# Kernel tuning notes

Measured on AMD Instinct MI355X. Metric: run time of the kernel, lower is better.

Reference implementation:

```python
import jax, jax.numpy as jnp
import numpy as np

EMBED_DIM = 1024
NUM_HEADS = 16
HEAD_DIM = EMBED_DIM // NUM_HEADS


def setup_inputs() -> dict:
    key = jax.random.key(0)
    ks = jax.random.split(key, 6)
    s = 1.0 / np.sqrt(EMBED_DIM)
    x = jax.random.normal(ks[0], (2, 2048, EMBED_DIM), dtype=jnp.float32)
    # torch Linear weights are [out, in]; y = x @ W.T
    Wq = jax.random.uniform(ks[1], (EMBED_DIM, EMBED_DIM), jnp.float32, -s, s)
    Wk = jax.random.uniform(ks[2], (EMBED_DIM, EMBED_DIM), jnp.float32, -s, s)
    Wv = jax.random.uniform(ks[3], (EMBED_DIM, EMBED_DIM), jnp.float32, -s, s)
    Wo = jax.random.uniform(ks[4], (EMBED_DIM, EMBED_DIM), jnp.float32, -s, s)
    bo = jax.random.uniform(ks[5], (EMBED_DIM,), jnp.float32, -s, s)
    return {"x": x, "Wq": Wq, "Wk": Wk, "Wv": Wv, "Wo": Wo, "bo": bo}


def reference(x, Wq, Wk, Wv, Wo, bo):
    B, T, C = x.shape
    H, D = NUM_HEADS, HEAD_DIM
    # projections (torch Linear: x @ W.T)
    Q = (x @ Wq.T).reshape(B, T, H, D).transpose(0, 2, 1, 3)  # [B,H,T,D]
    K = (x @ Wk.T).reshape(B, T, H, D).transpose(0, 2, 1, 3)
    V = (x @ Wv.T).reshape(B, T, H, D).transpose(0, 2, 1, 3)
    scores = jnp.einsum('bhqd,bhkd->bhqk', Q, K) / jnp.sqrt(jnp.float32(D))
    causal = jnp.tril(jnp.ones((T, T), dtype=bool))
    scores = jnp.where(causal, scores, -jnp.inf)
    weights = jax.nn.softmax(scores, axis=-1)  # dropout=0.0 (eval): identity
    out = jnp.einsum('bhqk,bhkd->bhqd', weights, V)
    out = out.transpose(0, 2, 1, 3).reshape(B, T, C)
    return out @ Wo.T + bo
```

## Files before the change

### kernel.cpp

```cpp
#include <hip/hip_runtime.h>
#include <stdint.h>

typedef unsigned short u16;
typedef __bf16 bf16x4 __attribute__((ext_vector_type(4)));
typedef __bf16 bf16x8 __attribute__((ext_vector_type(8)));
typedef float f32x4 __attribute__((ext_vector_type(4)));

#define EMBED 1024
#define NHEAD 16
#define HDIM  64
#define BATCH 2
#define SEQ   2048
#define MROWS 4096

__device__ __forceinline__ u16 f2bf(float f) {
  union { float f; uint32_t u; } v; v.f = f;
  uint32_t u = v.u;
  return (u16)((u + 0x7FFFu + ((u >> 16) & 1u)) >> 16);
}

__device__ __forceinline__ float exp2_fast(float x) {
  float r; asm("v_exp_f32 %0, %1" : "=v"(r) : "v"(x)); return r;
}

__device__ __forceinline__ void gload16(const void* g, void* l) {
  __builtin_amdgcn_global_load_lds(
      (__attribute__((address_space(1))) uint32_t*)g,
      (__attribute__((address_space(3))) uint32_t*)l, 16, 0, 0);
}

__global__ __launch_bounds__(256) void convert_all(
    const float* __restrict__ x,  const float* __restrict__ wq,
    const float* __restrict__ wk, const float* __restrict__ wv,
    const float* __restrict__ wo,
    u16* __restrict__ xb, u16* __restrict__ wqb, u16* __restrict__ wkb,
    u16* __restrict__ wvb, u16* __restrict__ wob)
{
  int i4 = (blockIdx.x * 256 + threadIdx.x) * 4;
  const float* src; u16* dst; int off;
  if      (i4 < 4194304) { src = x;  dst = xb;  off = i4; }
  else if (i4 < 5242880) { src = wq; dst = wqb; off = i4 - 4194304; }
  else if (i4 < 6291456) { src = wk; dst = wkb; off = i4 - 5242880; }
  else if (i4 < 7340032) { src = wv; dst = wvb; off = i4 - 6291456; }
  else                   { src = wo; dst = wob; off = i4 - 7340032; }
  float4 v = *(const float4*)&src[off];
  ushort4 u;
  u.x = f2bf(v.x); u.y = f2bf(v.y); u.z = f2bf(v.z); u.w = f2bf(v.w);
  *(ushort4*)&dst[off] = u;
}

__global__ __launch_bounds__(256) void gemm_qkv(
    const u16* __restrict__ Ab, const u16* __restrict__ Wq,
    const u16* __restrict__ Wk, const u16* __restrict__ Wv,
    u16* __restrict__ Qb, u16* __restrict__ Kb, u16* __restrict__ Vt)
{
  const int bid = blockIdx.x;
  const int wg = (bid & 7) * 96 + (bid >> 3);
  const int my = wg / 24, nx = wg % 24;
  const int mode = nx >> 3;
  const u16* Bw = (mode == 0) ? Wq : (mode == 1) ? Wk : Wv;
  const int m0 = my * 128, n0 = (nx & 7) * 128;

  __shared__ __align__(16) u16 As[2][128 * 32];
  __shared__ __align__(16) u16 Bs[2][128 * 32];
  const int tid = threadIdx.x;
  const int lane = tid & 63, wid = tid >> 6;
  const int c = lane & 15, g = lane >> 4;
  const int wm = wid >> 1, wn = wid & 1;

  f32x4 acc[4][4] = {};

  auto stage = [&](int buf, int kt) {
#pragma unroll
    for (int i = 0; i < 2; ++i) {
      int ch = tid + i * 256;
      int row = ch >> 2, col8 = (ch & 3) * 8;
      gload16(Ab + (m0 + row) * 1024 + kt * 32 + col8, &As[buf][ch * 8]);
      gload16(Bw + (n0 + row) * 1024 + kt * 32 + col8, &Bs[buf][ch * 8]);
    }
  };

  stage(0, 0);
  __syncthreads();

  for (int kt = 0; kt < 32; ++kt) {
    const int cur = kt & 1;
    if (kt < 31) stage(cur ^ 1, kt + 1);
    bf16x8 af[4], bfr[4];
#pragma unroll
    for (int mi = 0; mi < 4; ++mi)
      af[mi] = *(const bf16x8*)&As[cur][(wm * 64 + mi * 16 + c) * 32 + g * 8];
#pragma unroll
    for (int ni = 0; ni < 4; ++ni)
      bfr[ni] = *(const bf16x8*)&Bs[cur][(wn * 64 + ni * 16 + c) * 32 + g * 8];
#pragma unroll
    for (int mi = 0; mi < 4; ++mi)
#pragma unroll
      for (int ni = 0; ni < 4; ++ni)
        acc[mi][ni] = __builtin_amdgcn_mfma_f32_16x16x32_bf16(
            af[mi], bfr[ni], acc[mi][ni], 0, 0, 0);
    __syncthreads();
  }

  const int gm = m0 + wm * 64;
  const int gn = n0 + wn * 64;
  if (mode < 2) {
    u16* Out = (mode == 0) ? Qb : Kb;
    const float sc = (mode == 0) ? 0.18033688011112042f : 1.0f;
#pragma unroll
    for (int mi = 0; mi < 4; ++mi)
#pragma unroll
      for (int ni = 0; ni < 4; ++ni)
#pragma unroll
        for (int r = 0; r < 4; ++r) {
          int m = gm + mi * 16 + 4 * g + r;
          int n = gn + ni * 16 + c;
          int b = m >> 11, t = m & 2047, h = n >> 6, d = n & 63;
          Out[((b * NHEAD + h) * SEQ + t) * HDIM + d] = f2bf(acc[mi][ni][r] * sc);
        }
  } else {
#pragma unroll
    for (int mi = 0; mi < 4; ++mi)
#pragma unroll
      for (int ni = 0; ni < 4; ++ni) {
        int m = gm + mi * 16 + 4 * g;
        int n = gn + ni * 16 + c;
        int b = m >> 11, t = m & 2047, h = n >> 6, d = n & 63;
        int tl = t & 63;
        int tp = (t & ~63) + (tl >> 5) * 32 + ((tl >> 2) & 3) * 8
                 + ((tl >> 4) & 1) * 4;
        ushort4 pk;
        pk.x = f2bf(acc[mi][ni][0]);
        pk.y = f2bf(acc[mi][ni][1]);
        pk.z = f2bf(acc[mi][ni][2]);
        pk.w = f2bf(acc[mi][ni][3]);
        *(ushort4*)&Vt[((b * NHEAD + h) * HDIM + d) * SEQ + tp] = pk;
      }
  }
}

__global__ __launch_bounds__(256, 4) void attn(
    const u16* __restrict__ Qb, const u16* __restrict__ Kb,
    const u16* __restrict__ Vt, u16* __restrict__ Ob)
{
  const int bid = blockIdx.x;
  const int xcd = bid & 7, d = bid >> 3;
  const int p = d >> 5, s = d & 31;
  const int bh = xcd * 4 + p;
  const int sp = (s + (p >> 1) * 16) & 31;
  const int qt = (p & 1) ? sp : 31 - sp;
  const int b = bh >> 4, h = bh & 15;
  const int q0 = qt * 64;

  __shared__ __align__(16) u16 Ks[2][64 * 64];
  __shared__ __align__(16) u16 Vs[2][64 * 64];

  const int tid = threadIdx.x, lane = tid & 63, w = tid >> 6;
  const int c = lane & 15, g = lane >> 4;

  const u16* Qg = Qb + bh * SEQ * HDIM;
  const u16* Kg = Kb + bh * SEQ * HDIM;
  const u16* Vg = Vt + bh * HDIM * SEQ;

  bf16x8 qf[2];
#pragma unroll
  for (int kk = 0; kk < 2; ++kk)
    qf[kk] = *(const bf16x8*)&Qg[(q0 + w * 16 + c) * HDIM + kk * 32 + g * 8];

  f32x4 o[4] = {};
  float lacc = 0.f;

  auto stage = [&](int buf, int j) {
    const int k0 = j * 64;
#pragma unroll
    for (int i = 0; i < 2; ++i) {
      int ch = tid + i * 256;
      int row = ch >> 3, c8 = ch & 7;
      int sc8 = c8 ^ (row & 7);
      gload16(Kg + (k0 + row) * HDIM + sc8 * 8, &Ks[buf][ch * 8]);
      gload16(Vg + row * SEQ + k0 + sc8 * 8, &Vs[buf][ch * 8]);
    }
  };

  stage(0, 0);
  __syncthreads();

  for (int j = 0; j <= qt; ++j) {
    const int cur = j & 1;
    if (j < qt) stage(cur ^ 1, j + 1);
    const int k0 = j * 64;

    f32x4 st[4] = {};
    __builtin_amdgcn_s_setprio(1);
#pragma unroll
    for (int kk = 0; kk < 2; ++kk)
#pragma unroll
      for (int kvt = 0; kvt < 4; ++kvt) {
        const int R = kvt * 16 + c;
        bf16x8 kf = *(const bf16x8*)
            &Ks[cur][R * 64 + (((kk * 4 + g) ^ (R & 7)) * 8)];
        st[kvt] = __builtin_amdgcn_mfma_f32_16x16x32_bf16(kf, qf[kk], st[kvt], 0, 0, 0);
      }
    __builtin_amdgcn_s_setprio(0);

    if (j == qt) {
      const int qrow = q0 + w * 16 + c;
#pragma unroll
      for (int kvt = 0; kvt < 4; ++kvt)
#pragma unroll
        for (int r = 0; r < 4; ++r) {
          int kv = k0 + kvt * 16 + 4 * g + r;
          st[kvt][r] = (kv <= qrow) ? st[kvt][r] : -1e30f;
        }
    }

    bf16x8 pa[2];
#pragma unroll
    for (int kvt = 0; kvt < 4; ++kvt)
#pragma unroll
      for (int r = 0; r < 4; ++r) {
        float p2 = exp2_fast(st[kvt][r]);
        lacc += p2;
        pa[kvt >> 1][(kvt & 1) * 4 + r] = (__bf16)p2;
      }

    __builtin_amdgcn_s_setprio(1);
#pragma unroll
    for (int kk = 0; kk < 2; ++kk)
#pragma unroll
      for (int ni = 0; ni < 4; ++ni) {
        const int dd = ni * 16 + c;
        bf16x8 vf = *(const bf16x8*)
            &Vs[cur][dd * 64 + (((kk * 4 + g) ^ (dd & 7)) * 8)];
        o[ni] = __builtin_amdgcn_mfma_f32_16x16x32_bf16(pa[kk], vf, o[ni], 0, 0, 0);
      }
    __builtin_amdgcn_s_setprio(0);

    __syncthreads();
  }

  float rs = lacc;
  rs += __shfl_xor(rs, 16);
  rs += __shfl_xor(rs, 32);
  const float inv = 1.0f / rs;
  float lr[4];
#pragma unroll
  for (int r = 0; r < 4; ++r) lr[r] = __shfl(inv, 4 * g + r);
#pragma unroll
  for (int ni = 0; ni < 4; ++ni)
#pragma unroll
    for (int r = 0; r < 4; ++r) {
      int nc = h * HDIM + ni * 16 + c;
      int mr = b * SEQ + q0 + w * 16 + 4 * g + r;
      Ob[mr * EMBED + nc] = f2bf(o[ni][r] * lr[r]);
    }
}

__global__ __launch_bounds__(256) void gemm_out(
    const u16* __restrict__ Ab, const u16* __restrict__ Bw,
    const float* __restrict__ bias, float* __restrict__ Out)
{
  const int bid = blockIdx.x;
  const int wg = (bid & 7) * 64 + (bid >> 3);
  const int my = wg >> 3, nx = wg & 7;
  const int m0 = my * 64, n0 = nx * 128;

  __shared__ __align__(16) u16 As[2][64 * 32];
  __shared__ __align__(16) u16 Bs[2][128 * 32];
  const int tid = threadIdx.x;
  const int lane = tid & 63, wid = tid >> 6;
  const int c = lane & 15, g = lane >> 4;
  const int wm = wid >> 1, wn = wid & 1;

  f32x4 acc[2][4] = {};

  auto stage = [&](int buf, int kt) {
    {
      int ch = tid;
      int row = ch >> 2, col8 = (ch & 3) * 8;
      gload16(Ab + (m0 + row) * 1024 + kt * 32 + col8, &As[buf][ch * 8]);
    }
#pragma unroll
    for (int i = 0; i < 2; ++i) {
      int ch = tid + i * 256;
      int row = ch >> 2, col8 = (ch & 3) * 8;
      gload16(Bw + (n0 + row) * 1024 + kt * 32 + col8, &Bs[buf][ch * 8]);
    }
  };

  stage(0, 0);
  __syncthreads();

  for (int kt = 0; kt < 32; ++kt) {
    const int cur = kt & 1;
    if (kt < 31) stage(cur ^ 1, kt + 1);
    bf16x8 af[2], bfr[4];
#pragma unroll
    for (int mi = 0; mi < 2; ++mi)
      af[mi] = *(const bf16x8*)&As[cur][(wm * 32 + mi * 16 + c) * 32 + g * 8];
#pragma unroll
    for (int ni = 0; ni < 4; ++ni)
      bfr[ni] = *(const bf16x8*)&Bs[cur][(wn * 64 + ni * 16 + c) * 32 + g * 8];
#pragma unroll
    for (int mi = 0; mi < 2; ++mi)
#pragma unroll
      for (int ni = 0; ni < 4; ++ni)
        acc[mi][ni] = __builtin_amdgcn_mfma_f32_16x16x32_bf16(
            af[mi], bfr[ni], acc[mi][ni], 0, 0, 0);
    __syncthreads();
  }

  const int gm = m0 + wm * 32;
  const int gn = n0 + wn * 64;
#pragma unroll
  for (int mi = 0; mi < 2; ++mi)
#pragma unroll
    for (int ni = 0; ni < 4; ++ni)
#pragma unroll
      for (int r = 0; r < 4; ++r) {
        int m = gm + mi * 16 + 4 * g + r;
        int n = gn + ni * 16 + c;
        Out[m * 1024 + n] = acc[mi][ni][r] + bias[n];
      }
}

extern "C" void kernel_launch(void* const* d_in, const int* in_sizes, int n_in,
                              void* d_out, int out_size, void* d_ws, size_t ws_size,
                              hipStream_t stream) {
  const float* x  = (const float*)d_in[0];
  const float* Wq = (const float*)d_in[1];
  const float* Wk = (const float*)d_in[2];
  const float* Wv = (const float*)d_in[3];
  const float* Wo = (const float*)d_in[4];
  const float* bo = (const float*)d_in[5];
  char* ws = (char*)d_ws;
  u16* xb  = (u16*)(ws);
  u16* wqb = (u16*)(ws + 8388608);
  u16* wkb = (u16*)(ws + 10485760);
  u16* wvb = (u16*)(ws + 12582912);
  u16* wob = (u16*)(ws + 14680064);
  u16* Qb  = (u16*)(ws + 16777216);
  u16* Kb  = (u16*)(ws + 25165824);
  u16* Vt  = (u16*)(ws + 33554432);
  u16* Ob  = (u16*)(ws + 41943040);

  convert_all<<<8192, 256, 0, stream>>>(x, Wq, Wk, Wv, Wo,
                                        xb, wqb, wkb, wvb, wob);
  gemm_qkv<<<dim3(768), 256, 0, stream>>>(xb, wqb, wkb, wvb, Qb, Kb, Vt);
  attn<<<dim3(1024), 256, 0, stream>>>(Qb, Kb, Vt, Ob);
  gemm_out<<<dim3(512), 256, 0, stream>>>(Ob, wob, bo, (float*)d_out);
}
```

Baseline: 104.5 us.

## Double attention query tile to 128 rows per block to reuse K/V tiles

Each attention block now processes 128 query rows (two 16-row sub-tiles per wave) instead of 64, so every staged K/V tile in shared memory feeds twice the MFMA work. The grid is halved to 512 blocks, with a new mapping that pairs a short and a long causal query block per slot for load balancing. The cost is more registers per thread, so the occupancy hint is lowered from 4 to 2 blocks, and there are fewer blocks to spread across CUs.

```diff
diff --git a/kernel.cpp b/kernel.cpp
--- a/kernel.cpp
+++ b/kernel.cpp
@@ -139,18 +139,18 @@
   }
 }
 
-__global__ __launch_bounds__(256, 4) void attn(
+__global__ __launch_bounds__(256, 2) void attn(
     const u16* __restrict__ Qb, const u16* __restrict__ Kb,
     const u16* __restrict__ Vt, u16* __restrict__ Ob)
 {
   const int bid = blockIdx.x;
   const int xcd = bid & 7, d = bid >> 3;
-  const int p = d >> 5, s = d & 31;
-  const int bh = xcd * 4 + p;
-  const int sp = (s + (p >> 1) * 16) & 31;
-  const int qt = (p & 1) ? sp : 31 - sp;
+  const int s = d & 31, p = d >> 5;
+  const int bh = xcd * 4 + (s >> 3);
+  const int qb = p ? (15 - (s & 7)) : (s & 7);
   const int b = bh >> 4, h = bh & 15;
-  const int q0 = qt * 64;
+  const int q0 = qb * 128;
+  const int ntile = 2 * qb + 2;
 
   __shared__ __align__(16) u16 Ks[2][64 * 64];
   __shared__ __align__(16) u16 Vs[2][64 * 64];
@@ -162,13 +162,15 @@
   const u16* Kg = Kb + bh * SEQ * HDIM;
   const u16* Vg = Vt + bh * HDIM * SEQ;
 
-  bf16x8 qf[2];
-#pragma unroll
-  for (int kk = 0; kk < 2; ++kk)
-    qf[kk] = *(const bf16x8*)&Qg[(q0 + w * 16 + c) * HDIM + kk * 32 + g * 8];
-
-  f32x4 o[4] = {};
-  float lacc = 0.f;
+  bf16x8 qfA[2], qfB[2];
+#pragma unroll
+  for (int kk = 0; kk < 2; ++kk) {
+    qfA[kk] = *(const bf16x8*)&Qg[(q0 + w * 32 + c) * HDIM + kk * 32 + g * 8];
+    qfB[kk] = *(const bf16x8*)&Qg[(q0 + w * 32 + 16 + c) * HDIM + kk * 32 + g * 8];
+  }
+
+  f32x4 oA[4] = {}, oB[4] = {};
+  float laccA = 0.f, laccB = 0.f;
 
   auto stage = [&](int buf, int j) {
     const int k0 = j * 64;
@@ -185,12 +187,12 @@
   stage(0, 0);
   __syncthreads();
 
-  for (int j = 0; j <= qt; ++j) {
+  for (int j = 0; j < ntile; ++j) {
     const int cur = j & 1;
-    if (j < qt) stage(cur ^ 1, j + 1);
+    if (j + 1 < ntile) stage(cur ^ 1, j + 1);
     const int k0 = j * 64;
 
-    f32x4 st[4] = {};
+    f32x4 stA[4] = {}, stB[4] = {};
     __builtin_amdgcn_s_setprio(1);
 #pragma unroll
     for (int kk = 0; kk < 2; ++kk)
@@ -199,29 +201,35 @@
         const int R = kvt * 16 + c;
         bf16x8 kf = *(const bf16x8*)
             &Ks[cur][R * 64 + (((kk * 4 + g) ^ (R & 7)) * 8)];
-        st[kvt] = __builtin_amdgcn_mfma_f32_16x16x32_bf16(kf, qf[kk], st[kvt], 0, 0, 0);
+        stA[kvt] = __builtin_amdgcn_mfma_f32_16x16x32_bf16(kf, qfA[kk], stA[kvt], 0, 0, 0);
+        stB[kvt] = __builtin_amdgcn_mfma_f32_16x16x32_bf16(kf, qfB[kk], stB[kvt], 0, 0, 0);
       }
     __builtin_amdgcn_s_setprio(0);
 
-    if (j == qt) {
-      const int qrow = q0 + w * 16 + c;
+    if (j >= 2 * qb) {
+      const int qrowA = q0 + w * 32 + c;
+      const int qrowB = qrowA + 16;
 #pragma unroll
       for (int kvt = 0; kvt < 4; ++kvt)
 #pragma unroll
         for (int r = 0; r < 4; ++r) {
           int kv = k0 + kvt * 16 + 4 * g + r;
-          st[kvt][r] = (kv <= qrow) ? st[kvt][r] : -1e30f;
+          stA[kvt][r] = (kv <= qrowA) ? stA[kvt][r] : -1e30f;
+          stB[kvt][r] = (kv <= qrowB) ? stB[kvt][r] : -1e30f;
         }
     }
 
-    bf16x8 pa[2];
+    bf16x8 paA[2], paB[2];
 #pragma unroll
     for (int kvt = 0; kvt < 4; ++kvt)
 #pragma unroll
       for (int r = 0; r < 4; ++r) {
-        float p2 = exp2_fast(st[kvt][r]);
-        lacc += p2;
-        pa[kvt >> 1][(kvt & 1) * 4 + r] = (__bf16)p2;
+        float pA = exp2_fast(stA[kvt][r]);
+        laccA += pA;
+        paA[kvt >> 1][(kvt & 1) * 4 + r] = (__bf16)pA;
+        float pB = exp2_fast(stB[kvt][r]);
+        laccB += pB;
+        paB[kvt >> 1][(kvt & 1) * 4 + r] = (__bf16)pB;
       }
 
     __builtin_amdgcn_s_setprio(1);
@@ -232,27 +240,33 @@
         const int dd = ni * 16 + c;
         bf16x8 vf = *(const bf16x8*)
             &Vs[cur][dd * 64 + (((kk * 4 + g) ^ (dd & 7)) * 8)];
-        o[ni] = __builtin_amdgcn_mfma_f32_16x16x32_bf16(pa[kk], vf, o[ni], 0, 0, 0);
+        oA[ni] = __builtin_amdgcn_mfma_f32_16x16x32_bf16(paA[kk], vf, oA[ni], 0, 0, 0);
+        oB[ni] = __builtin_amdgcn_mfma_f32_16x16x32_bf16(paB[kk], vf, oB[ni], 0, 0, 0);
       }
     __builtin_amdgcn_s_setprio(0);
 
     __syncthreads();
   }
 
-  float rs = lacc;
-  rs += __shfl_xor(rs, 16);
-  rs += __shfl_xor(rs, 32);
-  const float inv = 1.0f / rs;
-  float lr[4];
-#pragma unroll
-  for (int r = 0; r < 4; ++r) lr[r] = __shfl(inv, 4 * g + r);
+  float rsA = laccA, rsB = laccB;
+  rsA += __shfl_xor(rsA, 16); rsA += __shfl_xor(rsA, 32);
+  rsB += __shfl_xor(rsB, 16); rsB += __shfl_xor(rsB, 32);
+  const float invA = 1.0f / rsA, invB = 1.0f / rsB;
+  float lrA[4], lrB[4];
+#pragma unroll
+  for (int r = 0; r < 4; ++r) {
+    lrA[r] = __shfl(invA, 4 * g + r);
+    lrB[r] = __shfl(invB, 4 * g + r);
+  }
 #pragma unroll
   for (int ni = 0; ni < 4; ++ni)
 #pragma unroll
     for (int r = 0; r < 4; ++r) {
       int nc = h * HDIM + ni * 16 + c;
-      int mr = b * SEQ + q0 + w * 16 + 4 * g + r;
-      Ob[mr * EMBED + nc] = f2bf(o[ni][r] * lr[r]);
+      int mrA = b * SEQ + q0 + w * 32 + 4 * g + r;
+      Ob[mrA * EMBED + nc] = f2bf(oA[ni][r] * lrA[r]);
+      int mrB = b * SEQ + q0 + w * 32 + 16 + 4 * g + r;
+      Ob[mrB * EMBED + nc] = f2bf(oB[ni][r] * lrB[r]);
     }
 }
 
@@ -347,6 +361,6 @@
   convert_all<<<8192, 256, 0, stream>>>(x, Wq, Wk, Wv, Wo,
                                         xb, wqb, wkb, wvb, wob);
   gemm_qkv<<<dim3(768), 256, 0, stream>>>(xb, wqb, wkb, wvb, Qb, Kb, Vt);
-  attn<<<dim3(1024), 256, 0, stream>>>(Qb, Kb, Vt, Ob);
+  attn<<<dim3(512), 256, 0, stream>>>(Qb, Kb, Vt, Ob);
   gemm_out<<<dim3(512), 256, 0, stream>>>(Ob, wob, bo, (float*)d_out);
 }
```

Result: slower. 106.7 us (+2.1%).

## Load K/V fragments directly from global memory, dropping LDS double buffering

Applied to the files above, without the earlier changes.

Removes the shared-memory double-buffered staging of K and V tiles and the per-iteration block barrier. Each wave now loads its MFMA operand fragments for K and V straight from global memory into registers. This removes LDS traffic and synchronisation, but each of the four waves fetches the same K/V data separately. That leans on the L1/L2 caches, loses explicit prefetch of the next tile, and exposes global-load latency inside the loop.

```diff
diff --git a/kernel.cpp b/kernel.cpp
--- a/kernel.cpp
+++ b/kernel.cpp
@@ -152,9 +152,6 @@
   const int b = bh >> 4, h = bh & 15;
   const int q0 = qt * 64;
 
-  __shared__ __align__(16) u16 Ks[2][64 * 64];
-  __shared__ __align__(16) u16 Vs[2][64 * 64];
-
   const int tid = threadIdx.x, lane = tid & 63, w = tid >> 6;
   const int c = lane & 15, g = lane >> 4;
 
@@ -170,38 +167,35 @@
   f32x4 o[4] = {};
   float lacc = 0.f;
 
-  auto stage = [&](int buf, int j) {
+  const u16* Kp = Kg + c * HDIM + g * 8;
+  const u16* Vp = Vg + c * SEQ + g * 8;
+
+  for (int j = 0; j <= qt; ++j) {
     const int k0 = j * 64;
-#pragma unroll
-    for (int i = 0; i < 2; ++i) {
-      int ch = tid + i * 256;
-      int row = ch >> 3, c8 = ch & 7;
-      int sc8 = c8 ^ (row & 7);
-      gload16(Kg + (k0 + row) * HDIM + sc8 * 8, &Ks[buf][ch * 8]);
-      gload16(Vg + row * SEQ + k0 + sc8 * 8, &Vs[buf][ch * 8]);
-    }
-  };
-
-  stage(0, 0);
-  __syncthreads();
-
-  for (int j = 0; j <= qt; ++j) {
-    const int cur = j & 1;
-    if (j < qt) stage(cur ^ 1, j + 1);
-    const int k0 = j * 64;
+
+    bf16x8 kf[2][4];
+#pragma unroll
+    for (int kk = 0; kk < 2; ++kk)
+#pragma unroll
+      for (int kvt = 0; kvt < 4; ++kvt)
+        kf[kk][kvt] = *(const bf16x8*)&Kp[(k0 + kvt * 16) * HDIM + kk * 32];
 
     f32x4 st[4] = {};
     __builtin_amdgcn_s_setprio(1);
 #pragma unroll
     for (int kk = 0; kk < 2; ++kk)
 #pragma unroll
-      for (int kvt = 0; kvt < 4; ++kvt) {
-        const int R = kvt * 16 + c;
-        bf16x8 kf = *(const bf16x8*)
-            &Ks[cur][R * 64 + (((kk * 4 + g) ^ (R & 7)) * 8)];
-        st[kvt] = __builtin_amdgcn_mfma_f32_16x16x32_bf16(kf, qf[kk], st[kvt], 0, 0, 0);
-      }
+      for (int kvt = 0; kvt < 4; ++kvt)
+        st[kvt] = __builtin_amdgcn_mfma_f32_16x16x32_bf16(
+            kf[kk][kvt], qf[kk], st[kvt], 0, 0, 0);
     __builtin_amdgcn_s_setprio(0);
+
+    bf16x8 vfr[2][4];
+#pragma unroll
+    for (int kk = 0; kk < 2; ++kk)
+#pragma unroll
+      for (int ni = 0; ni < 4; ++ni)
+        vfr[kk][ni] = *(const bf16x8*)&Vp[ni * 16 * SEQ + k0 + kk * 32];
 
     if (j == qt) {
       const int qrow = q0 + w * 16 + c;
@@ -228,15 +222,10 @@
 #pragma unroll
     for (int kk = 0; kk < 2; ++kk)
 #pragma unroll
-      for (int ni = 0; ni < 4; ++ni) {
-        const int dd = ni * 16 + c;
-        bf16x8 vf = *(const bf16x8*)
-            &Vs[cur][dd * 64 + (((kk * 4 + g) ^ (dd & 7)) * 8)];
-        o[ni] = __builtin_amdgcn_mfma_f32_16x16x32_bf16(pa[kk], vf, o[ni], 0, 0, 0);
-      }
+      for (int ni = 0; ni < 4; ++ni)
+        o[ni] = __builtin_amdgcn_mfma_f32_16x16x32_bf16(
+            pa[kk], vfr[kk][ni], o[ni], 0, 0, 0);
     __builtin_amdgcn_s_setprio(0);
-
-    __syncthreads();
   }
 
   float rs = lacc;
```

New measurement: 187.5 us. 79.5% more time.

## Fuse x fp32-to-bf16 conversion into QKV GEMM via fp32 LDS staging

Applied to the files above, without the earlier changes.

Drops the separate conversion pass over the activation x. The QKV GEMM now stages fp32 tiles of x into LDS with an XOR swizzle and converts them to bf16 in registers before the MFMA. This removes one full write and read of a bf16 copy of x. In exchange the GEMM reads twice the bytes of x per tile from global memory across 24 column blocks, uses double the LDS for A, and does extra conversion ALU work inside the main loop. Conversion now uses the compiler's __bf16 cast instead of the manual rounding.

```diff
diff --git a/kernel.cpp b/kernel.cpp
--- a/kernel.cpp
+++ b/kernel.cpp
@@ -29,20 +29,18 @@
       (__attribute__((address_space(3))) uint32_t*)l, 16, 0, 0);
 }
 
-__global__ __launch_bounds__(256) void convert_all(
-    const float* __restrict__ x,  const float* __restrict__ wq,
-    const float* __restrict__ wk, const float* __restrict__ wv,
-    const float* __restrict__ wo,
-    u16* __restrict__ xb, u16* __restrict__ wqb, u16* __restrict__ wkb,
+__global__ __launch_bounds__(256) void convert_w(
+    const float* __restrict__ wq, const float* __restrict__ wk,
+    const float* __restrict__ wv, const float* __restrict__ wo,
+    u16* __restrict__ wqb, u16* __restrict__ wkb,
     u16* __restrict__ wvb, u16* __restrict__ wob)
 {
   int i4 = (blockIdx.x * 256 + threadIdx.x) * 4;
   const float* src; u16* dst; int off;
-  if      (i4 < 4194304) { src = x;  dst = xb;  off = i4; }
-  else if (i4 < 5242880) { src = wq; dst = wqb; off = i4 - 4194304; }
-  else if (i4 < 6291456) { src = wk; dst = wkb; off = i4 - 5242880; }
-  else if (i4 < 7340032) { src = wv; dst = wvb; off = i4 - 6291456; }
-  else                   { src = wo; dst = wob; off = i4 - 7340032; }
+  if      (i4 < 1048576) { src = wq; dst = wqb; off = i4; }
+  else if (i4 < 2097152) { src = wk; dst = wkb; off = i4 - 1048576; }
+  else if (i4 < 3145728) { src = wv; dst = wvb; off = i4 - 2097152; }
+  else                   { src = wo; dst = wob; off = i4 - 3145728; }
   float4 v = *(const float4*)&src[off];
   ushort4 u;
   u.x = f2bf(v.x); u.y = f2bf(v.y); u.z = f2bf(v.z); u.w = f2bf(v.w);
@@ -50,7 +48,7 @@
 }
 
 __global__ __launch_bounds__(256) void gemm_qkv(
-    const u16* __restrict__ Ab, const u16* __restrict__ Wq,
+    const float* __restrict__ Ax, const u16* __restrict__ Wq,
     const u16* __restrict__ Wk, const u16* __restrict__ Wv,
     u16* __restrict__ Qb, u16* __restrict__ Kb, u16* __restrict__ Vt)
 {
@@ -61,8 +59,8 @@
   const u16* Bw = (mode == 0) ? Wq : (mode == 1) ? Wk : Wv;
   const int m0 = my * 128, n0 = (nx & 7) * 128;
 
-  __shared__ __align__(16) u16 As[2][128 * 32];
-  __shared__ __align__(16) u16 Bs[2][128 * 32];
+  __shared__ __align__(16) float As[2][128 * 32];
+  __shared__ __align__(16) u16  Bs[2][128 * 32];
   const int tid = threadIdx.x;
   const int lane = tid & 63, wid = tid >> 6;
   const int c = lane & 15, g = lane >> 4;
@@ -72,10 +70,16 @@
 
   auto stage = [&](int buf, int kt) {
 #pragma unroll
+    for (int i = 0; i < 4; ++i) {
+      int ch = tid + i * 256;
+      int row = ch >> 3, c8 = ch & 7;
+      int sc8 = c8 ^ (row & 7);
+      gload16(Ax + (m0 + row) * 1024 + kt * 32 + sc8 * 4, &As[buf][ch * 4]);
+    }
+#pragma unroll
     for (int i = 0; i < 2; ++i) {
       int ch = tid + i * 256;
       int row = ch >> 2, col8 = (ch & 3) * 8;
-      gload16(Ab + (m0 + row) * 1024 + kt * 32 + col8, &As[buf][ch * 8]);
       gload16(Bw + (n0 + row) * 1024 + kt * 32 + col8, &Bs[buf][ch * 8]);
     }
   };
@@ -88,8 +92,17 @@
     if (kt < 31) stage(cur ^ 1, kt + 1);
     bf16x8 af[4], bfr[4];
 #pragma unroll
-    for (int mi = 0; mi < 4; ++mi)
-      af[mi] = *(const bf16x8*)&As[cur][(wm * 64 + mi * 16 + c) * 32 + g * 8];
+    for (int mi = 0; mi < 4; ++mi) {
+      const int row = wm * 64 + mi * 16 + c;
+      f32x4 lo = *(const f32x4*)&As[cur][row * 32 + (((2 * g) ^ (row & 7)) * 4)];
+      f32x4 hi = *(const f32x4*)&As[cur][row * 32 + (((2 * g + 1) ^ (row & 7)) * 4)];
+      bf16x8 a;
+      a[0] = (__bf16)lo[0]; a[1] = (__bf16)lo[1];
+      a[2] = (__bf16)lo[2]; a[3] = (__bf16)lo[3];
+      a[4] = (__bf16)hi[0]; a[5] = (__bf16)hi[1];
+      a[6] = (__bf16)hi[2]; a[7] = (__bf16)hi[3];
+      af[mi] = a;
+    }
 #pragma unroll
     for (int ni = 0; ni < 4; ++ni)
       bfr[ni] = *(const bf16x8*)&Bs[cur][(wn * 64 + ni * 16 + c) * 32 + g * 8];
@@ -334,7 +347,6 @@
   const float* Wo = (const float*)d_in[4];
   const float* bo = (const float*)d_in[5];
   char* ws = (char*)d_ws;
-  u16* xb  = (u16*)(ws);
   u16* wqb = (u16*)(ws + 8388608);
   u16* wkb = (u16*)(ws + 10485760);
   u16* wvb = (u16*)(ws + 12582912);
@@ -344,9 +356,8 @@
   u16* Vt  = (u16*)(ws + 33554432);
   u16* Ob  = (u16*)(ws + 41943040);
 
-  convert_all<<<8192, 256, 0, stream>>>(x, Wq, Wk, Wv, Wo,
-                                        xb, wqb, wkb, wvb, wob);
-  gemm_qkv<<<dim3(768), 256, 0, stream>>>(xb, wqb, wkb, wvb, Qb, Kb, Vt);
+  convert_w<<<4096, 256, 0, stream>>>(Wq, Wk, Wv, Wo, wqb, wkb, wvb, wob);
+  gemm_qkv<<<dim3(768), 256, 0, stream>>>(x, wqb, wkb, wvb, Qb, Kb, Vt);
   attn<<<dim3(1024), 256, 0, stream>>>(Qb, Kb, Vt, Ob);
   gemm_out<<<dim3(512), 256, 0, stream>>>(Ob, wob, bo, (float*)d_out);
 }
```

New measurement: 110.4 us. 1.06x slower.
